# Kernel tuning notes

Hardware: AMD Instinct MI355X
Metric: run time of the kernel (lower is better)

Reference implementation:

```python
import jax, jax.numpy as jnp
import numpy as np

T, D, N, H = 2032, 1408, 16, 88  # K == N (MHA vision attention)
BLOCK_SIZE = 128
ROPE_THETA = 10000.0


def _apply_rope_interleaved(x_tnh, freqs_cis):
    # x_tnh: [T, N, H]; freqs_cis: [T, H//2, 2] with (..., 0)=cos, (..., 1)=sin.
    cos = freqs_cis[:, None, :, 0]  # [T, 1, H//2]
    sin = freqs_cis[:, None, :, 1]
    x1 = x_tnh[..., 0::2]
    x2 = x_tnh[..., 1::2]
    # interleaved rotation: pairs (even, odd) rotated by angle theta_t
    rot = jnp.stack([x1 * cos - x2 * sin, x1 * sin + x2 * cos], axis=-1)
    return rot.reshape(x_tnh.shape)


def setup_inputs() -> dict:
    key = jax.random.key(0)
    ks = jax.random.split(key, 10)
    s = 0.02
    x = jax.random.normal(ks[0], (T, D), dtype=jnp.float32)
    # precomputed rotary cos/sin table (interleaved ordering)
    pos = jnp.arange(T, dtype=jnp.float32)
    inv_freq = ROPE_THETA ** (-jnp.arange(0, H, 2, dtype=jnp.float32) / H)  # [H//2]
    ang = pos[:, None] * inv_freq[None, :]                                  # [T, H//2]
    freqs_cis = jnp.stack([jnp.cos(ang), jnp.sin(ang)], axis=-1)            # [T, H//2, 2]
    Wq = jax.random.normal(ks[1], (D, N, H), dtype=jnp.float32) * s
    Wk = jax.random.normal(ks[2], (D, N, H), dtype=jnp.float32) * s
    Wv = jax.random.normal(ks[3], (D, N, H), dtype=jnp.float32) * s
    Wo = jax.random.normal(ks[4], (N, H, D), dtype=jnp.float32) * s
    bq = jax.random.normal(ks[5], (N, H), dtype=jnp.float32) * s
    bk = jax.random.normal(ks[6], (N, H), dtype=jnp.float32) * s
    bv = jax.random.normal(ks[7], (N, H), dtype=jnp.float32) * s
    bo = jax.random.normal(ks[8], (D,), dtype=jnp.float32) * s
    return {"x": x, "freqs_cis": freqs_cis, "Wq": Wq, "bq": bq, "Wk": Wk,
            "bk": bk, "Wv": Wv, "bv": bv, "Wo": Wo, "bo": bo}


def reference(x, freqs_cis, Wq, bq, Wk, bk, Wv, bv, Wo, bo):
    t, d = x.shape
    n, h = bq.shape
    sm_scale = h ** -0.5
    # fused QKV projections + bias + RoPE (q, k only)
    q = jnp.einsum('td,dnh->tnh', x, Wq) + bq[None]
    q = _apply_rope_interleaved(q, freqs_cis)
    k = jnp.einsum('td,dkh->tkh', x, Wk) + bk[None]
    k = _apply_rope_interleaved(k, freqs_cis)
    v = jnp.einsum('td,dkh->tkh', x, Wv) + bv[None]
    # pad T up to a multiple of BLOCK_SIZE, as the flash-attention call requires
    pad_len = (BLOCK_SIZE - t % BLOCK_SIZE) % BLOCK_SIZE
    qp = jnp.pad(q, ((0, pad_len), (0, 0), (0, 0)))
    kp = jnp.pad(k, ((0, pad_len), (0, 0), (0, 0)))
    vp = jnp.pad(v, ((0, pad_len), (0, 0), (0, 0)))
    # [N, Tp, H]
    qh = jnp.transpose(qp, (1, 0, 2))
    kh = jnp.transpose(kp, (1, 0, 2))
    vh = jnp.transpose(vp, (1, 0, 2))
    # segment ids: 0 for valid tokens, 1 for padding; attention only within equal ids
    seg = jnp.concatenate([jnp.zeros((t,), jnp.int32), jnp.ones((pad_len,), jnp.int32)])
    mask = seg[:, None] == seg[None, :]  # [Tp, Tp]
    scores = jnp.einsum('nth,nsh->nts', qh, kh) * sm_scale
    scores = jnp.where(mask[None], scores, jnp.finfo(scores.dtype).min)
    probs = jax.nn.softmax(scores, axis=-1)
    out = jnp.einsum('nts,nsh->nth', probs, vh)        # [N, Tp, H]
    out = jnp.transpose(out, (1, 0, 2))[:t]            # [T, N, H]
    o = jnp.einsum('tnh,nhd->td', out, Wo) + bo
    return o
```

## Files before the change

### kernel.cpp

```cpp
#include <hip/hip_runtime.h>
#include <hip/hip_bf16.h>
#include <stdint.h>
#include <stddef.h>

typedef __bf16 bf16_t;
typedef __bf16 bf16x8 __attribute__((ext_vector_type(8)));
typedef __bf16 bf16x4 __attribute__((ext_vector_type(4)));
typedef __bf16 bf16x2 __attribute__((ext_vector_type(2)));
typedef float  f32x4  __attribute__((ext_vector_type(4)));

#define T_SEQ 2032
#define T_PAD 2048
#define DM    1408
#define NHEAD 16
#define HD    88
#define HP    96
#define VST   2112
#define KVB   64
#define NT    (T_PAD / KVB)
#define SM_SCALE 0.10660035817780521f
#define LOG2E 1.4426950408889634f
#define DEFER_THR 8.0f

__device__ __forceinline__ void gload_lds16(const bf16_t* g, bf16_t* l) {
  __builtin_amdgcn_global_load_lds(
      (__attribute__((address_space(1))) void*)(g),
      (__attribute__((address_space(3))) void*)(l), 16, 0, 0);
}

__global__ void k_convert_x(const float* __restrict__ x, bf16_t* __restrict__ Xb) {
  int idx = blockIdx.x * 256 + threadIdx.x;
  const int total = T_PAD * DM / 4;
  if (idx >= total) return;
  int base = idx * 4;
  int t = base / DM;
  float4 v;
  if (t < T_SEQ) v = *(const float4*)(x + base);
  else           v = make_float4(0.f, 0.f, 0.f, 0.f);
  bf16x4 o;
  o[0] = (bf16_t)v.x; o[1] = (bf16_t)v.y; o[2] = (bf16_t)v.z; o[3] = (bf16_t)v.w;
  *(bf16x4*)(Xb + base) = o;
}

__global__ void k_transpose4(const float* __restrict__ W0, const float* __restrict__ W1,
                             const float* __restrict__ W2, const float* __restrict__ W3,
                             bf16_t* __restrict__ d012, bf16_t* __restrict__ d3) {
  const int which = blockIdx.x / 484;
  const int b = blockIdx.x % 484;
  const float* src = (which == 0) ? W0 : (which == 1) ? W1 : (which == 2) ? W2 : W3;
  bf16_t* dst = (which < 3) ? (d012 + (size_t)which * DM * DM) : d3;
  const int tr = b / 22, tc = b % 22;
  __shared__ float tile[64][65];
  const int t = threadIdx.x;
  const int row = t >> 2, l4 = t & 3;
#pragma unroll
  for (int i = 0; i < 4; ++i) {
    float4 v = *(const float4*)(src + (size_t)(tr * 64 + row) * DM + tc * 64 + l4 * 16 + i * 4);
    *(float4*)&tile[row][l4 * 16 + i * 4] = v;
  }
  __syncthreads();
  const int jj = t >> 2;
#pragma unroll
  for (int it = 0; it < 2; ++it) {
    const int c = (t & 3) + 4 * it;
    bf16x8 o;
#pragma unroll
    for (int e = 0; e < 8; ++e) o[e] = (bf16_t)tile[c * 8 + e][jj];
    *(bf16x8*)(dst + (size_t)(tc * 64 + jj) * DM + tr * 64 + c * 8) = o;
  }
}

__device__ __forceinline__ void gemm_main_1408(
    const bf16_t* __restrict__ A, const bf16_t* __restrict__ Bt,
    bf16_t* As, bf16_t* Bs, int m0, int n0, f32x4 acc[4][4]) {
  const int tid = threadIdx.x;
  const int w = tid >> 6, lane = tid & 63;
  const int l15 = lane & 15, lg = lane >> 4;
  const int b0 = w * 2048 + lane * 16;
  const int r0 = b0 >> 6, k0 = (b0 & 63) >> 1;
  const int b1 = b0 + 1024;
  const int r1 = b1 >> 6, k1 = (b1 & 63) >> 1;
  const int wr = w >> 1, wc = w & 1;
  const size_t aoff0 = (size_t)(m0 + r0) * DM + k0;
  const size_t aoff1 = (size_t)(m0 + r1) * DM + k1;
  const size_t boff0 = (size_t)(n0 + r0) * DM + k0;
  const size_t boff1 = (size_t)(n0 + r1) * DM + k1;
  gload_lds16(A + aoff0, As + w * 1024);
  gload_lds16(A + aoff1, As + w * 1024 + 512);
  gload_lds16(Bt + boff0, Bs + w * 1024);
  gload_lds16(Bt + boff1, Bs + w * 1024 + 512);
  for (int kt = 0; kt < 44; ++kt) {
    const int cur = kt & 1;
    const int kon = ((kt < 43) ? kt + 1 : 43) * 32;
    const int db = (cur ^ 1) * 4096;
    gload_lds16(A + aoff0 + kon, As + db + w * 1024);
    gload_lds16(A + aoff1 + kon, As + db + w * 1024 + 512);
    gload_lds16(Bt + boff0 + kon, Bs + db + w * 1024);
    gload_lds16(Bt + boff1 + kon, Bs + db + w * 1024 + 512);
    asm volatile("s_waitcnt vmcnt(4)" ::: "memory");
    __builtin_amdgcn_s_barrier();
    const bf16_t* Ac = As + cur * 4096;
    const bf16_t* Bc = Bs + cur * 4096;
    bf16x8 av[4], bv[4];
#pragma unroll
    for (int m = 0; m < 4; ++m)
      av[m] = *(const bf16x8*)(Ac + (wr * 64 + m * 16 + l15) * 32 + lg * 8);
#pragma unroll
    for (int n = 0; n < 4; ++n)
      bv[n] = *(const bf16x8*)(Bc + (wc * 64 + n * 16 + l15) * 32 + lg * 8);
    __builtin_amdgcn_s_setprio(1);
#pragma unroll
    for (int m = 0; m < 4; ++m)
#pragma unroll
      for (int n = 0; n < 4; ++n)
        acc[m][n] = __builtin_amdgcn_mfma_f32_16x16x32_bf16(av[m], bv[n], acc[m][n], 0, 0, 0);
    __builtin_amdgcn_s_setprio(0);
    __builtin_amdgcn_s_barrier();
  }
  asm volatile("s_waitcnt vmcnt(0)" ::: "memory");
}

__global__ __launch_bounds__(256, 3) void k_gemm_qkv(
    const bf16_t* __restrict__ A, const bf16_t* __restrict__ Bt,
    const float* __restrict__ bq, const float* __restrict__ bk,
    const float* __restrict__ bvp, const float* __restrict__ freqs,
    bf16_t* __restrict__ Qh, bf16_t* __restrict__ Kh, bf16_t* __restrict__ Vt) {
  __shared__ bf16_t As[2 * 4096];
  __shared__ bf16_t Bs[2 * 4096];
  const int bid = blockIdx.x;
  const int sbid = (bid & 7) * 66 + (bid >> 3);
  const int mt = sbid / 33, nt = sbid % 33;
  f32x4 acc[4][4];
#pragma unroll
  for (int m = 0; m < 4; ++m)
#pragma unroll
    for (int n = 0; n < 4; ++n) acc[m][n] = (f32x4){0.f, 0.f, 0.f, 0.f};
  gemm_main_1408(A, Bt, As, Bs, mt * 128, nt * 128, acc);
  const int tid = threadIdx.x, w = tid >> 6, lane = tid & 63;
  const int l15 = lane & 15, lg = lane >> 4;
  const int wr = w >> 1, wc = w & 1;
  const int cb = nt * 128 + wc * 64, rb = mt * 128 + wr * 64;
#pragma unroll
  for (int n = 0; n < 4; ++n) {
    const int col = cb + n * 16 + l15;
    const int seg = (col >= 2 * DM) ? 2 : ((col >= DM) ? 1 : 0);
    const int cc = col - seg * DM;
    const float* bp = (seg == 0) ? bq : (seg == 1) ? bk : bvp;
    const float bval = bp[cc];
    const int hn = cc / 88;
    const int hh = cc - hn * 88;
    const int hbase = hh & ~1;
    const bool odd = hh & 1;
#pragma unroll
    for (int m = 0; m < 4; ++m) {
      const int tb = rb + m * 16 + lg * 4;
      if (seg == 2) {
        bf16x4 vv;
#pragma unroll
        for (int r = 0; r < 4; ++r) vv[r] = (bf16_t)(acc[m][n][r] + bval);
        *(bf16x4*)(Vt + ((size_t)hn * HP + hh) * VST + tb) = vv;
      } else {
#pragma unroll
        for (int r = 0; r < 4; ++r) {
          const int t = tb + r;
          const float v = acc[m][n][r] + bval;
          const float p = __shfl_xor(v, 1);
          const int tc2 = (t < T_SEQ) ? t : 0;
          const float c = freqs[tc2 * 88 + hbase];
          const float s = freqs[tc2 * 88 + hbase + 1];
          const float x1 = odd ? p : v;
          const float x2 = odd ? v : p;
          const float ro = odd ? (x1 * s + x2 * c) : (x1 * c - x2 * s);
          if (seg == 0)
            Qh[((size_t)hn * T_PAD + t) * HP + hh] = (bf16_t)(ro * (SM_SCALE * LOG2E));
          else
            Kh[((size_t)hn * T_PAD + t) * HP + hh] = (bf16_t)ro;
        }
      }
    }
  }
}

__global__ __launch_bounds__(256, 3) void k_gemm_out64(
    const bf16_t* __restrict__ A, const bf16_t* __restrict__ Bt,
    const float* __restrict__ bo, float* __restrict__ out) {
  __shared__ bf16_t Sm[2 * 4096];
  const int bid = blockIdx.x;
  const int sbid = (bid & 7) * 88 + (bid >> 3);
  const int mt = sbid / 22, nt = sbid % 22;
  const int m0 = mt * 64, n0 = nt * 64;
  const int tid = threadIdx.x, w = tid >> 6, lane = tid & 63;
  const int l15 = lane & 15, lg = lane >> 4;
  const int wr = w >> 1, wc = w & 1;
  const bf16_t* srcp[2];
  size_t srco[2];
  int dste[2];
#pragma unroll
  for (int p = 0; p < 2; ++p) {
    const int off = (w * 2 + p) * 1024;
    const int o = off + lane * 16;
    dste[p] = off >> 1;
    if (off < 4096) {
      int r = o >> 6, k = (o & 63) >> 1;
      srcp[p] = A; srco[p] = (size_t)(m0 + r) * DM + k;
    } else {
      int ob = o - 4096;
      int r = ob >> 6, k = (ob & 63) >> 1;
      srcp[p] = Bt; srco[p] = (size_t)(n0 + r) * DM + k;
    }
  }
  f32x4 acc[2][2];
#pragma unroll
  for (int m = 0; m < 2; ++m)
#pragma unroll
    for (int n = 0; n < 2; ++n) acc[m][n] = (f32x4){0.f, 0.f, 0.f, 0.f};
#pragma unroll
  for (int p = 0; p < 2; ++p) gload_lds16(srcp[p] + srco[p], Sm + dste[p]);
  for (int kt = 0; kt < 44; ++kt) {
    const int cur = kt & 1;
    const int kon = ((kt < 43) ? kt + 1 : 43) * 32;
    const int db = (cur ^ 1) * 4096;
#pragma unroll
    for (int p = 0; p < 2; ++p)
      gload_lds16(srcp[p] + srco[p] + kon, Sm + db + dste[p]);
    asm volatile("s_waitcnt vmcnt(2)" ::: "memory");
    __builtin_amdgcn_s_barrier();
    const bf16_t* Sc = Sm + cur * 4096;
    bf16x8 av[2], bv2[2];
#pragma unroll
    for (int m = 0; m < 2; ++m)
      av[m] = *(const bf16x8*)(Sc + (wr * 32 + m * 16 + l15) * 32 + lg * 8);
#pragma unroll
    for (int n = 0; n < 2; ++n)
      bv2[n] = *(const bf16x8*)(Sc + 2048 + (wc * 32 + n * 16 + l15) * 32 + lg * 8);
    __builtin_amdgcn_s_setprio(1);
#pragma unroll
    for (int m = 0; m < 2; ++m)
#pragma unroll
      for (int n = 0; n < 2; ++n)
        acc[m][n] = __builtin_amdgcn_mfma_f32_16x16x32_bf16(av[m], bv2[n], acc[m][n], 0, 0, 0);
    __builtin_amdgcn_s_setprio(0);
    __builtin_amdgcn_s_barrier();
  }
  asm volatile("s_waitcnt vmcnt(0)" ::: "memory");
#pragma unroll
  for (int n = 0; n < 2; ++n) {
    const int col = n0 + wc * 32 + n * 16 + l15;
    const float bval = bo[col];
#pragma unroll
    for (int m = 0; m < 2; ++m) {
#pragma unroll
      for (int r = 0; r < 4; ++r) {
        const int t = m0 + wr * 32 + m * 16 + lg * 4 + r;
        if (t < T_SEQ) out[(size_t)t * DM + col] = acc[m][n][r] + bval;
      }
    }
  }
}

__global__ __launch_bounds__(256, 2) void k_attn(
    const bf16_t* __restrict__ Qh, const bf16_t* __restrict__ Kh,
    const bf16_t* __restrict__ Vt, bf16_t* __restrict__ Ob) {
  __shared__ bf16_t Ks[2][KVB * 128];
  __shared__ bf16_t Ps[4][16 * 72];
  const int tid = threadIdx.x;
  const int w = tid >> 6, lane = tid & 63;
  const int l15 = lane & 15, lg = lane >> 4;
  const int swz = l15 & 7;
  const int bid = blockIdx.x;
  const int sbid = (bid & 7) * 64 + (bid >> 3);
  const int head = sbid >> 5;
  const int qt = sbid & 31;
  const bf16_t* Qn = Qh + (size_t)head * T_PAD * HP;
  const bf16_t* Kn = Kh + (size_t)head * T_PAD * HP;
  const bf16_t* Vn = Vt + (size_t)head * HP * VST;
  const int q0 = qt * 64 + w * 16;

  bf16x8 qf[3];
#pragma unroll
  for (int kh = 0; kh < 3; ++kh)
    qf[kh] = *(const bf16x8*)(Qn + (size_t)(q0 + l15) * HP + kh * 32 + lg * 8);

  f32x4 oacc[6];
#pragma unroll
  for (int j = 0; j < 6; ++j) oacc[j] = (f32x4){0.f, 0.f, 0.f, 0.f};
  float mrow = -1e30f;
  float lrowp = 0.f;

  int kro[4], kco[4];
#pragma unroll
  for (int p = 0; p < 4; ++p) {
    int o = (w * 4 + p) * 1024 + lane * 16;
    int row = o >> 8, ch = (o >> 4) & 15;
    kro[p] = row; kco[p] = (ch ^ (row & 7)) << 3;
  }
#pragma unroll
  for (int p = 0; p < 4; ++p)
    gload_lds16(Kn + (size_t)kro[p] * HP + kco[p], &Ks[0][(w * 4 + p) * 512]);

  for (int kvt = 0; kvt < NT; ++kvt) {
    const int s0 = kvt * KVB;
    const int cur = kvt & 1;
    const int nxt = (kvt < NT - 1) ? kvt + 1 : kvt;
#pragma unroll
    for (int p = 0; p < 4; ++p)
      gload_lds16(Kn + (size_t)(nxt * KVB + kro[p]) * HP + kco[p],
                  &Ks[cur ^ 1][(w * 4 + p) * 512]);
    asm volatile("s_waitcnt vmcnt(4)" ::: "memory");
    __builtin_amdgcn_s_barrier();

    const bf16_t* Kc = Ks[cur];
    f32x4 sf[4];
    __builtin_amdgcn_s_setprio(1);
#pragma unroll
    for (int ss = 0; ss < 4; ++ss) {
      f32x4 s = {0.f, 0.f, 0.f, 0.f};
#pragma unroll
      for (int kh = 0; kh < 3; ++kh) {
        bf16x8 kf = *(const bf16x8*)(Kc + (ss * 16 + l15) * 128 + (((kh * 4 + lg) ^ swz) << 3));
        s = __builtin_amdgcn_mfma_f32_16x16x32_bf16(kf, qf[kh], s, 0, 0, 0);
      }
      sf[ss] = s;
    }
    __builtin_amdgcn_s_setprio(0);
    bf16x8 vf[12];
#pragma unroll
    for (int ks = 0; ks < 2; ++ks)
#pragma unroll
      for (int j = 0; j < 6; ++j)
        vf[ks * 6 + j] = *(const bf16x8*)(
            Vn + (size_t)(j * 16 + l15) * VST + s0 + ks * 32 + lg * 8);
    if (s0 + KVB > T_SEQ) {
#pragma unroll
      for (int ss = 0; ss < 4; ++ss)
#pragma unroll
        for (int r = 0; r < 4; ++r)
          if (s0 + ss * 16 + lg * 4 + r >= T_SEQ) sf[ss][r] = -1e30f;
    }
    float tm = sf[0][0];
#pragma unroll
    for (int ss = 0; ss < 4; ++ss)
#pragma unroll
      for (int r = 0; r < 4; ++r) tm = fmaxf(tm, sf[ss][r]);
    tm = fmaxf(tm, __shfl_xor(tm, 16));
    tm = fmaxf(tm, __shfl_xor(tm, 32));
    if (!__all(tm <= mrow + DEFER_THR)) {
      const float mn = fmaxf(mrow, tm);
      const float scv = __builtin_amdgcn_exp2f(mrow - mn);
      mrow = mn;
      lrowp *= scv;
#pragma unroll
      for (int r = 0; r < 4; ++r) {
        const float sq = __shfl(scv, lg * 4 + r, 16);
#pragma unroll
        for (int j = 0; j < 6; ++j) oacc[j][r] *= sq;
      }
    }
    float rs = 0.f;
#pragma unroll
    for (int ss = 0; ss < 4; ++ss)
#pragma unroll
      for (int jj = 0; jj < 2; ++jj) {
        const float p0 = __builtin_amdgcn_exp2f(sf[ss][2 * jj] - mrow);
        const float p1 = __builtin_amdgcn_exp2f(sf[ss][2 * jj + 1] - mrow);
        rs += p0 + p1;
        bf16x2 pk; pk[0] = (bf16_t)p0; pk[1] = (bf16_t)p1;
        *(bf16x2*)(&Ps[w][l15 * 72 + ss * 16 + lg * 4 + 2 * jj]) = pk;
      }
    lrowp += rs;
    __builtin_amdgcn_s_setprio(1);
#pragma unroll
    for (int ks = 0; ks < 2; ++ks) {
      bf16x8 pa = *(const bf16x8*)(&Ps[w][l15 * 72 + ks * 32 + lg * 8]);
#pragma unroll
      for (int j = 0; j < 6; ++j)
        oacc[j] = __builtin_amdgcn_mfma_f32_16x16x32_bf16(pa, vf[ks * 6 + j], oacc[j], 0, 0, 0);
    }
    __builtin_amdgcn_s_setprio(0);
    __builtin_amdgcn_s_barrier();
  }
  asm volatile("s_waitcnt vmcnt(0)" ::: "memory");

  lrowp += __shfl_xor(lrowp, 16);
  lrowp += __shfl_xor(lrowp, 32);
  float lq[4];
#pragma unroll
  for (int r = 0; r < 4; ++r) lq[r] = __shfl(lrowp, lg * 4 + r, 16);
#pragma unroll
  for (int j = 0; j < 6; ++j) {
    const int h = j * 16 + l15;
    if (h < HD) {
#pragma unroll
      for (int r = 0; r < 4; ++r) {
        const int t = q0 + lg * 4 + r;
        if (t < T_SEQ)
          Ob[(size_t)t * DM + head * HD + h] = (bf16_t)(oacc[j][r] / lq[r]);
      }
    }
  }
}

extern "C" void kernel_launch(void* const* d_in, const int* in_sizes, int n_in,
                              void* d_out, int out_size, void* d_ws, size_t ws_size,
                              hipStream_t stream) {
  (void)in_sizes; (void)n_in; (void)out_size;
  const float* x     = (const float*)d_in[0];
  const float* freqs = (const float*)d_in[1];
  const float* Wq    = (const float*)d_in[2];
  const float* bq    = (const float*)d_in[3];
  const float* Wk    = (const float*)d_in[4];
  const float* bk    = (const float*)d_in[5];
  const float* Wv    = (const float*)d_in[6];
  const float* bv    = (const float*)d_in[7];
  const float* Wo    = (const float*)d_in[8];
  const float* bo    = (const float*)d_in[9];
  float* out = (float*)d_out;
  char* ws = (char*)d_ws;

  bf16_t* Xb  = (bf16_t*)(ws);
  bf16_t* Wt  = (bf16_t*)(ws + 5767168);
  bf16_t* Qh  = (bf16_t*)(ws + 17661952);
  bf16_t* Kh  = (bf16_t*)(ws + 23953408);
  bf16_t* Vt  = (bf16_t*)(ws + 30244864);
  bf16_t* Ob  = Xb;
  const size_t NEED_ALL = 36732928ull + 3964928ull;
  const bool sep_wot = (ws_size >= NEED_ALL);
  bf16_t* Wot = sep_wot ? (bf16_t*)(ws + 36732928) : Wt;

  hipMemsetAsync(Qh, 0, 6291456, stream);

  k_convert_x<<<(T_PAD * DM / 4 + 255) / 256, 256, 0, stream>>>(x, Xb);
  if (sep_wot) {
    k_transpose4<<<4 * 484, 256, 0, stream>>>(Wq, Wk, Wv, Wo, Wt, Wot);
  } else {
    k_transpose4<<<3 * 484, 256, 0, stream>>>(Wq, Wk, Wv, Wo, Wt, Wot);
  }

  k_gemm_qkv<<<16 * 33, 256, 0, stream>>>(Xb, Wt, bq, bk, bv, freqs, Qh, Kh, Vt);

  if (!sep_wot)
    k_transpose4<<<484, 256, 0, stream>>>(Wo, Wo, Wo, Wo, Wot, Wot);

  k_attn<<<NHEAD * 32, 256, 0, stream>>>(Qh, Kh, Vt, Ob);
  k_gemm_out64<<<32 * 22, 256, 0, stream>>>(Ob, Wot, bo, out);
}
```

Measured before the change: 277.9 us.

## Split attention KV across waves with 32-row query tiles and LDS merge

```diff
diff --git a/kernel.cpp b/kernel.cpp
--- a/kernel.cpp
+++ b/kernel.cpp
@@ -16,8 +16,6 @@
 #define HD    88
 #define HP    96
 #define VST   2112
-#define KVB   64
-#define NT    (T_PAD / KVB)
 #define SM_SCALE 0.10660035817780521f
 #define LOG2E 1.4426950408889634f
 #define DEFER_THR 8.0f
@@ -258,143 +256,201 @@
   }
 }
 
-__global__ __launch_bounds__(256, 2) void k_attn(
+__global__ __launch_bounds__(256, 3) void k_attn(
     const bf16_t* __restrict__ Qh, const bf16_t* __restrict__ Kh,
     const bf16_t* __restrict__ Vt, bf16_t* __restrict__ Ob) {
-  __shared__ bf16_t Ks[2][KVB * 128];
-  __shared__ bf16_t Ps[4][16 * 72];
+  __shared__ bf16_t Ks[128 * 128];
+  __shared__ bf16_t Ps[4][2][640];
   const int tid = threadIdx.x;
   const int w = tid >> 6, lane = tid & 63;
   const int l15 = lane & 15, lg = lane >> 4;
   const int swz = l15 & 7;
   const int bid = blockIdx.x;
-  const int sbid = (bid & 7) * 64 + (bid >> 3);
-  const int head = sbid >> 5;
-  const int qt = sbid & 31;
+  const int sbid = (bid & 7) * 128 + (bid >> 3);
+  const int head = sbid >> 6;
+  const int qt = sbid & 63;
   const bf16_t* Qn = Qh + (size_t)head * T_PAD * HP;
   const bf16_t* Kn = Kh + (size_t)head * T_PAD * HP;
   const bf16_t* Vn = Vt + (size_t)head * HP * VST;
-  const int q0 = qt * 64 + w * 16;
-
-  bf16x8 qf[3];
-#pragma unroll
-  for (int kh = 0; kh < 3; ++kh)
-    qf[kh] = *(const bf16x8*)(Qn + (size_t)(q0 + l15) * HP + kh * 32 + lg * 8);
-
-  f32x4 oacc[6];
-#pragma unroll
-  for (int j = 0; j < 6; ++j) oacc[j] = (f32x4){0.f, 0.f, 0.f, 0.f};
-  float mrow = -1e30f;
-  float lrowp = 0.f;
-
-  int kro[4], kco[4];
-#pragma unroll
-  for (int p = 0; p < 4; ++p) {
-    int o = (w * 4 + p) * 1024 + lane * 16;
+  const int q0 = qt * 32;
+
+  bf16x8 qf[2][3];
+#pragma unroll
+  for (int qb = 0; qb < 2; ++qb)
+#pragma unroll
+    for (int kh = 0; kh < 3; ++kh)
+      qf[qb][kh] = *(const bf16x8*)(Qn + (size_t)(q0 + qb * 16 + l15) * HP + kh * 32 + lg * 8);
+
+  f32x4 oacc[2][6];
+#pragma unroll
+  for (int qb = 0; qb < 2; ++qb)
+#pragma unroll
+    for (int j = 0; j < 6; ++j) oacc[qb][j] = (f32x4){0.f, 0.f, 0.f, 0.f};
+  float m[2] = {-1e30f, -1e30f};
+  float l[2] = {0.f, 0.f};
+
+  int ksrc[8];
+#pragma unroll
+  for (int p = 0; p < 8; ++p) {
+    int o = (w * 8 + p) * 1024 + lane * 16;
     int row = o >> 8, ch = (o >> 4) & 15;
-    kro[p] = row; kco[p] = (ch ^ (row & 7)) << 3;
-  }
-#pragma unroll
-  for (int p = 0; p < 4; ++p)
-    gload_lds16(Kn + (size_t)kro[p] * HP + kco[p], &Ks[0][(w * 4 + p) * 512]);
-
-  for (int kvt = 0; kvt < NT; ++kvt) {
-    const int s0 = kvt * KVB;
-    const int cur = kvt & 1;
-    const int nxt = (kvt < NT - 1) ? kvt + 1 : kvt;
-#pragma unroll
-    for (int p = 0; p < 4; ++p)
-      gload_lds16(Kn + (size_t)(nxt * KVB + kro[p]) * HP + kco[p],
-                  &Ks[cur ^ 1][(w * 4 + p) * 512]);
-    asm volatile("s_waitcnt vmcnt(4)" ::: "memory");
+    ksrc[p] = row * HP + ((ch ^ (row & 7)) << 3);
+  }
+
+  for (int t = 0; t < 16; ++t) {
+    const int s0 = t * 128;
+#pragma unroll
+    for (int p = 0; p < 8; ++p)
+      gload_lds16(Kn + (size_t)s0 * HP + ksrc[p], Ks + (w * 8 + p) * 512);
+    __builtin_amdgcn_sched_barrier(0);
+    bf16x8 vf[6];
+#pragma unroll
+    for (int j = 0; j < 6; ++j)
+      vf[j] = *(const bf16x8*)(Vn + (size_t)(j * 16 + l15) * VST + s0 + w * 32 + lg * 8);
+    __builtin_amdgcn_sched_barrier(0);
+    asm volatile("s_waitcnt vmcnt(6)" ::: "memory");
     __builtin_amdgcn_s_barrier();
 
-    const bf16_t* Kc = Ks[cur];
-    f32x4 sf[4];
+    f32x4 sf[2][2];
+#pragma unroll
+    for (int qb = 0; qb < 2; ++qb)
+#pragma unroll
+      for (int ss = 0; ss < 2; ++ss) sf[qb][ss] = (f32x4){0.f, 0.f, 0.f, 0.f};
     __builtin_amdgcn_s_setprio(1);
 #pragma unroll
-    for (int ss = 0; ss < 4; ++ss) {
-      f32x4 s = {0.f, 0.f, 0.f, 0.f};
+    for (int ss = 0; ss < 2; ++ss)
 #pragma unroll
       for (int kh = 0; kh < 3; ++kh) {
-        bf16x8 kf = *(const bf16x8*)(Kc + (ss * 16 + l15) * 128 + (((kh * 4 + lg) ^ swz) << 3));
-        s = __builtin_amdgcn_mfma_f32_16x16x32_bf16(kf, qf[kh], s, 0, 0, 0);
-      }
-      sf[ss] = s;
-    }
+        bf16x8 kf = *(const bf16x8*)(
+            Ks + (w * 32 + ss * 16 + l15) * 128 + (((kh * 4 + lg) ^ swz) << 3));
+        sf[0][ss] = __builtin_amdgcn_mfma_f32_16x16x32_bf16(kf, qf[0][kh], sf[0][ss], 0, 0, 0);
+        sf[1][ss] = __builtin_amdgcn_mfma_f32_16x16x32_bf16(kf, qf[1][kh], sf[1][ss], 0, 0, 0);
+      }
     __builtin_amdgcn_s_setprio(0);
-    bf16x8 vf[12];
-#pragma unroll
-    for (int ks = 0; ks < 2; ++ks)
-#pragma unroll
-      for (int j = 0; j < 6; ++j)
-        vf[ks * 6 + j] = *(const bf16x8*)(
-            Vn + (size_t)(j * 16 + l15) * VST + s0 + ks * 32 + lg * 8);
-    if (s0 + KVB > T_SEQ) {
-#pragma unroll
-      for (int ss = 0; ss < 4; ++ss)
+    if (s0 + 128 > T_SEQ) {
+#pragma unroll
+      for (int ss = 0; ss < 2; ++ss)
 #pragma unroll
         for (int r = 0; r < 4; ++r)
-          if (s0 + ss * 16 + lg * 4 + r >= T_SEQ) sf[ss][r] = -1e30f;
-    }
-    float tm = sf[0][0];
-#pragma unroll
-    for (int ss = 0; ss < 4; ++ss)
-#pragma unroll
-      for (int r = 0; r < 4; ++r) tm = fmaxf(tm, sf[ss][r]);
-    tm = fmaxf(tm, __shfl_xor(tm, 16));
-    tm = fmaxf(tm, __shfl_xor(tm, 32));
-    if (!__all(tm <= mrow + DEFER_THR)) {
-      const float mn = fmaxf(mrow, tm);
-      const float scv = __builtin_amdgcn_exp2f(mrow - mn);
-      mrow = mn;
-      lrowp *= scv;
-#pragma unroll
-      for (int r = 0; r < 4; ++r) {
-        const float sq = __shfl(scv, lg * 4 + r, 16);
-#pragma unroll
-        for (int j = 0; j < 6; ++j) oacc[j][r] *= sq;
-      }
-    }
-    float rs = 0.f;
-#pragma unroll
-    for (int ss = 0; ss < 4; ++ss)
-#pragma unroll
-      for (int jj = 0; jj < 2; ++jj) {
-        const float p0 = __builtin_amdgcn_exp2f(sf[ss][2 * jj] - mrow);
-        const float p1 = __builtin_amdgcn_exp2f(sf[ss][2 * jj + 1] - mrow);
-        rs += p0 + p1;
-        bf16x2 pk; pk[0] = (bf16_t)p0; pk[1] = (bf16_t)p1;
-        *(bf16x2*)(&Ps[w][l15 * 72 + ss * 16 + lg * 4 + 2 * jj]) = pk;
-      }
-    lrowp += rs;
+          if (s0 + w * 32 + ss * 16 + lg * 4 + r >= T_SEQ) {
+            sf[0][ss][r] = -1e30f; sf[1][ss][r] = -1e30f;
+          }
+    }
+    float tm[2];
+#pragma unroll
+    for (int qb = 0; qb < 2; ++qb) {
+      float v = fmaxf(fmaxf(sf[qb][0][0], sf[qb][0][1]), fmaxf(sf[qb][0][2], sf[qb][0][3]));
+      v = fmaxf(v, fmaxf(fmaxf(sf[qb][1][0], sf[qb][1][1]), fmaxf(sf[qb][1][2], sf[qb][1][3])));
+      v = fmaxf(v, __shfl_xor(v, 16));
+      v = fmaxf(v, __shfl_xor(v, 32));
+      tm[qb] = v;
+    }
+    if (!__all((tm[0] <= m[0] + DEFER_THR) && (tm[1] <= m[1] + DEFER_THR))) {
+#pragma unroll
+      for (int qb = 0; qb < 2; ++qb) {
+        const float mn = fmaxf(m[qb], tm[qb]);
+        const float scv = __builtin_amdgcn_exp2f(m[qb] - mn);
+        m[qb] = mn;
+        l[qb] *= scv;
+#pragma unroll
+        for (int r = 0; r < 4; ++r) {
+          const float sq = __shfl(scv, lg * 4 + r, 16);
+#pragma unroll
+          for (int j = 0; j < 6; ++j) oacc[qb][j][r] *= sq;
+        }
+      }
+    }
+#pragma unroll
+    for (int qb = 0; qb < 2; ++qb) {
+      float rs = 0.f;
+#pragma unroll
+      for (int ss = 0; ss < 2; ++ss)
+#pragma unroll
+        for (int jj = 0; jj < 2; ++jj) {
+          const float p0 = __builtin_amdgcn_exp2f(sf[qb][ss][2 * jj] - m[qb]);
+          const float p1 = __builtin_amdgcn_exp2f(sf[qb][ss][2 * jj + 1] - m[qb]);
+          rs += p0 + p1;
+          bf16x2 pk; pk[0] = (bf16_t)p0; pk[1] = (bf16_t)p1;
+          *(bf16x2*)(&Ps[w][qb][l15 * 40 + ss * 16 + lg * 4 + 2 * jj]) = pk;
+        }
+      l[qb] += rs;
+    }
+    asm volatile("s_waitcnt vmcnt(0)" ::: "memory");
+    bf16x8 pa0 = *(const bf16x8*)(&Ps[w][0][l15 * 40 + lg * 8]);
+    bf16x8 pa1 = *(const bf16x8*)(&Ps[w][1][l15 * 40 + lg * 8]);
     __builtin_amdgcn_s_setprio(1);
 #pragma unroll
-    for (int ks = 0; ks < 2; ++ks) {
-      bf16x8 pa = *(const bf16x8*)(&Ps[w][l15 * 72 + ks * 32 + lg * 8]);
-#pragma unroll
-      for (int j = 0; j < 6; ++j)
-        oacc[j] = __builtin_amdgcn_mfma_f32_16x16x32_bf16(pa, vf[ks * 6 + j], oacc[j], 0, 0, 0);
+    for (int j = 0; j < 6; ++j) {
+      oacc[0][j] = __builtin_amdgcn_mfma_f32_16x16x32_bf16(pa0, vf[j], oacc[0][j], 0, 0, 0);
+      oacc[1][j] = __builtin_amdgcn_mfma_f32_16x16x32_bf16(pa1, vf[j], oacc[1][j], 0, 0, 0);
     }
     __builtin_amdgcn_s_setprio(0);
     __builtin_amdgcn_s_barrier();
   }
   asm volatile("s_waitcnt vmcnt(0)" ::: "memory");
 
-  lrowp += __shfl_xor(lrowp, 16);
-  lrowp += __shfl_xor(lrowp, 32);
-  float lq[4];
-#pragma unroll
-  for (int r = 0; r < 4; ++r) lq[r] = __shfl(lrowp, lg * 4 + r, 16);
-#pragma unroll
-  for (int j = 0; j < 6; ++j) {
-    const int h = j * 16 + l15;
-    if (h < HD) {
-#pragma unroll
-      for (int r = 0; r < 4; ++r) {
-        const int t = q0 + lg * 4 + r;
-        if (t < T_SEQ)
-          Ob[(size_t)t * DM + head * HD + h] = (bf16_t)(oacc[j][r] / lq[r]);
+#pragma unroll
+  for (int qb = 0; qb < 2; ++qb) {
+    l[qb] += __shfl_xor(l[qb], 16);
+    l[qb] += __shfl_xor(l[qb], 32);
+  }
+
+  float* MB = (float*)Ks;
+  for (int p = 1; p < 4; ++p) {
+    if (w == p) {
+#pragma unroll
+      for (int qb = 0; qb < 2; ++qb) {
+#pragma unroll
+        for (int j = 0; j < 6; ++j)
+#pragma unroll
+          for (int r = 0; r < 4; ++r)
+            MB[((qb * 6 + j) * 4 + r) * 64 + lane] = oacc[qb][j][r];
+        MB[3072 + qb * 64 + lane] = m[qb];
+        MB[3200 + qb * 64 + lane] = l[qb];
+      }
+    }
+    __syncthreads();
+    if (w == 0) {
+#pragma unroll
+      for (int qb = 0; qb < 2; ++qb) {
+        const float mp = MB[3072 + qb * 64 + lane];
+        const float lp = MB[3200 + qb * 64 + lane];
+        const float mn = fmaxf(m[qb], mp);
+        const float wa = __builtin_amdgcn_exp2f(m[qb] - mn);
+        const float wb = __builtin_amdgcn_exp2f(mp - mn);
+        m[qb] = mn;
+        l[qb] = l[qb] * wa + lp * wb;
+#pragma unroll
+        for (int r = 0; r < 4; ++r) {
+          const float swa = __shfl(wa, lg * 4 + r, 16);
+          const float swb = __shfl(wb, lg * 4 + r, 16);
+#pragma unroll
+          for (int j = 0; j < 6; ++j)
+            oacc[qb][j][r] = oacc[qb][j][r] * swa +
+                             MB[((qb * 6 + j) * 4 + r) * 64 + lane] * swb;
+        }
+      }
+    }
+    __syncthreads();
+  }
+
+  if (w == 0) {
+#pragma unroll
+    for (int qb = 0; qb < 2; ++qb) {
+      float lq[4];
+#pragma unroll
+      for (int r = 0; r < 4; ++r) lq[r] = __shfl(l[qb], lg * 4 + r, 16);
+#pragma unroll
+      for (int j = 0; j < 6; ++j) {
+        const int h = j * 16 + l15;
+        if (h < HD) {
+#pragma unroll
+          for (int r = 0; r < 4; ++r) {
+            const int t = q0 + qb * 16 + lg * 4 + r;
+            if (t < T_SEQ)
+              Ob[(size_t)t * DM + head * HD + h] = (bf16_t)(oacc[qb][j][r] / lq[r]);
+          }
+        }
       }
     }
   }
@@ -441,6 +497,6 @@
   if (!sep_wot)
     k_transpose4<<<484, 256, 0, stream>>>(Wo, Wo, Wo, Wo, Wot, Wot);
 
-  k_attn<<<NHEAD * 32, 256, 0, stream>>>(Qh, Kh, Vt, Ob);
+  k_attn<<<16 * 64, 256, 0, stream>>>(Qh, Kh, Vt, Ob);
   k_gemm_out64<<<32 * 22, 256, 0, stream>>>(Ob, Wot, bo, out);
 }
```

Measured after the change: 255.7 us. 1.09x faster.
